# Kernel optimization log

Hardware: AMD Instinct MI355X
Metric: run time of the kernel (lower is better)

The kernel has to match this reference:

```python
import jax, jax.numpy as jnp
import numpy as np

LOC_SCOPE = 3.0
LOC_BIN_SIZE = 0.5
NUM_HEAD_BIN = 12
PER_LOC_BIN = int(LOC_SCOPE / LOC_BIN_SIZE) * 2  # 12
REG_C = PER_LOC_BIN * 4 + 1 + NUM_HEAD_BIN * 2 + 3  # 76


def decode_bbox_target(roi, reg, anchor):
    # roi: (M, 3) point centers; reg: (M, 76); anchor: (3,)
    b = PER_LOC_BIN
    f32 = reg.dtype
    x_bin = jnp.argmax(reg[:, 0:b], axis=1)
    z_bin = jnp.argmax(reg[:, b:2 * b], axis=1)
    pos_x = x_bin.astype(f32) * LOC_BIN_SIZE + LOC_BIN_SIZE / 2 - LOC_SCOPE
    pos_z = z_bin.astype(f32) * LOC_BIN_SIZE + LOC_BIN_SIZE / 2 - LOC_SCOPE
    # fine xz residual: gather residual of the argmax bin (batch_dims=1 gather)
    x_res = jnp.take_along_axis(reg[:, 2 * b:3 * b], x_bin[:, None], axis=1)[:, 0] * LOC_BIN_SIZE
    z_res = jnp.take_along_axis(reg[:, 3 * b:4 * b], z_bin[:, None], axis=1)[:, 0] * LOC_BIN_SIZE
    pos_x = pos_x + x_res
    pos_z = pos_z + z_res
    start = 4 * b
    # y by direct offset (get_y_by_bin=False)
    pos_y = roi[:, 1] + reg[:, start]
    start = start + 1
    # heading: coarse bin argmax + fine residual gather (get_ry_fine=False)
    ry_bin = jnp.argmax(reg[:, start:start + NUM_HEAD_BIN], axis=1)
    ry_res_norm = jnp.take_along_axis(
        reg[:, start + NUM_HEAD_BIN:start + 2 * NUM_HEAD_BIN], ry_bin[:, None], axis=1)[:, 0]
    angle_per_class = 2.0 * np.pi / NUM_HEAD_BIN
    ry = (ry_bin.astype(f32) * angle_per_class + ry_res_norm * (angle_per_class / 2)) % (2.0 * np.pi)
    ry = jnp.where(ry > np.pi, ry - 2.0 * np.pi, ry)
    # size: residual around anchor
    hwl = reg[:, start + 2 * NUM_HEAD_BIN:start + 2 * NUM_HEAD_BIN + 3] * anchor + anchor
    # roi has 3 cols -> no rotate_pc_along_y branch; shift x,z by roi center
    box = jnp.concatenate([
        (pos_x + roi[:, 0])[:, None],
        pos_y[:, None],
        (pos_z + roi[:, 2])[:, None],
        hwl,
        ry[:, None],
    ], axis=1)  # (M, 7)
    return box


def setup_inputs() -> dict:
    key = jax.random.key(0)
    k1, k2, k3 = jax.random.split(key, 3)
    B, N = 8, 131072
    rpn_scores = jax.random.normal(k1, (B, N), dtype=jnp.float32)
    rpn_reg = jax.random.normal(k2, (B, N, REG_C), dtype=jnp.float32)
    xyz = jax.random.normal(k3, (B, N, 3), dtype=jnp.float32) * 20.0
    anchor_size = jnp.array([1.52563191462, 1.62856739989, 3.88311640418], dtype=jnp.float32)
    return {"rpn_scores": rpn_scores, "rpn_reg": rpn_reg, "xyz": xyz, "anchor_size": anchor_size}


def reference(rpn_scores, rpn_reg, xyz, anchor_size):
    B, N, C = rpn_reg.shape
    props = decode_bbox_target(xyz.reshape(-1, 3), rpn_reg.reshape(-1, C), anchor_size)
    props = props.reshape(B, N, 7)
    # post_process: lift y to box top-center (y + h/2)
    props = jnp.concatenate([props[..., :1], props[..., 1:2] + props[..., 3:4] / 2, props[..., 2:]], axis=-1)
    # score-descending ordering of proposals (per batch row)
    order = jnp.argsort(-rpn_scores, axis=1)  # (B, N)
    boxes = jnp.take_along_axis(props, order[..., None], axis=1)
    scores = jnp.take_along_axis(rpn_scores, order, axis=1)
    # pack boxes+scores: (B, N, 8)
    return jnp.concatenate([boxes, scores[..., None]], axis=-1)
```

## Files before the change

### kernel.cpp

```cpp
#include <hip/hip_runtime.h>
#include <math.h>

#define N_PER   131072
#define NBATCH  8
#define REGC    76
#define TOTAL   (NBATCH * N_PER)
#define TILE    4096
#define NBLKSEG 32
#define BINS    256

__device__ __forceinline__ unsigned desc_key(float f) {
    unsigned u = __float_as_uint(f);
    return (u & 0x80000000u) ? u : ~(u | 0x80000000u);
}

__global__ __launch_bounds__(256) void decode_kernel(
    const float* __restrict__ scores, const float* __restrict__ reg,
    const float* __restrict__ xyz, const float* __restrict__ anchor,
    float* __restrict__ boxes8, unsigned* __restrict__ keyA,
    unsigned* __restrict__ payA)
{
    int p = blockIdx.x * 256 + threadIdx.x;
    const float* r = reg + (size_t)p * REGC;
    const float4* r4 = (const float4*)r;

    float4 q0 = r4[0],  q1 = r4[1],  q2 = r4[2];
    float4 q3 = r4[3],  q4 = r4[4],  q5 = r4[5];
    float4 s0 = r4[12], s1 = r4[13], s2 = r4[14], s3 = r4[15];
    float4 tt = r4[18];

    float xa[12] = {q0.x,q0.y,q0.z,q0.w, q1.x,q1.y,q1.z,q1.w, q2.x,q2.y,q2.z,q2.w};
    float za[12] = {q3.x,q3.y,q3.z,q3.w, q4.x,q4.y,q4.z,q4.w, q5.x,q5.y,q5.z,q5.w};
    float ra[12] = {s0.y,s0.z,s0.w, s1.x,s1.y,s1.z,s1.w, s2.x,s2.y,s2.z,s2.w, s3.x};

    int xb = 0; float xm = xa[0];
#pragma unroll
    for (int c = 1; c < 12; ++c) { if (xa[c] > xm) { xm = xa[c]; xb = c; } }
    int zb = 0; float zm = za[0];
#pragma unroll
    for (int c = 1; c < 12; ++c) { if (za[c] > zm) { zm = za[c]; zb = c; } }
    int yb = 0; float ym = ra[0];
#pragma unroll
    for (int c = 1; c < 12; ++c) { if (ra[c] > ym) { ym = ra[c]; yb = c; } }

    float x_res  = r[24 + xb];
    float z_res  = r[36 + zb];
    float ry_res = r[61 + yb];

    float rx = xyz[(size_t)p * 3 + 0];
    float ryy = xyz[(size_t)p * 3 + 1];
    float rz = xyz[(size_t)p * 3 + 2];
    float a0 = anchor[0], a1 = anchor[1], a2 = anchor[2];

    const float APC    = (float)(2.0 * M_PI / 12.0);
    const float HAPC   = (float)(M_PI / 12.0);
    const float TWO_PI = (float)(2.0 * M_PI);
    const float PI_F   = (float)M_PI;

    float vry = __fadd_rn(__fmul_rn((float)yb, APC), __fmul_rn(ry_res, HAPC));
    float m = fmodf(vry, TWO_PI);
    if (m < 0.0f) m += TWO_PI;
    if (m > PI_F) m -= TWO_PI;

    float h = tt.y * a0 + a0;
    float w = tt.z * a1 + a1;
    float l = tt.w * a2 + a2;

    float ox = (((float)xb * 0.5f + 0.25f - 3.0f) + x_res * 0.5f) + rx;
    float oz = (((float)zb * 0.5f + 0.25f - 3.0f) + z_res * 0.5f) + rz;
    float oy = (ryy + s0.x) + h * 0.5f;

    float sc = scores[p];

    float4* ob = (float4*)(boxes8 + (size_t)p * 8);
    ob[0] = make_float4(ox, oy, oz, h);
    ob[1] = make_float4(w, l, m, sc);

    keyA[p] = desc_key(sc);
    payA[p] = (unsigned)(p & (N_PER - 1));
}

__global__ __launch_bounds__(256) void hist_kernel(
    const unsigned* __restrict__ keyIn, unsigned* __restrict__ hist, int shift)
{
    __shared__ unsigned h[BINS];
    int tid = threadIdx.x;
    h[tid] = 0;
    __syncthreads();
    int seg = blockIdx.y, blk = blockIdx.x;
    const unsigned* k = keyIn + (size_t)seg * N_PER + (size_t)blk * TILE;
#pragma unroll
    for (int c = 0; c < TILE / 256; ++c) {
        unsigned d = (k[c * 256 + tid] >> shift) & 255u;
        atomicAdd(&h[d], 1u);
    }
    __syncthreads();
    hist[(size_t)(seg * BINS + tid) * NBLKSEG + blk] = h[tid];
}

__global__ __launch_bounds__(256) void scan_kernel(unsigned* __restrict__ hist)
{
    int seg = blockIdx.x, bin = threadIdx.x;
    unsigned* hp = hist + (size_t)(seg * BINS + bin) * NBLKSEG;
    unsigned run = 0;
#pragma unroll
    for (int blk = 0; blk < NBLKSEG; ++blk) {
        unsigned c = hp[blk];
        hp[blk] = run;
        run += c;
    }
    __shared__ unsigned sc[BINS];
    sc[bin] = run;
    __syncthreads();
    for (int off = 1; off < BINS; off <<= 1) {
        unsigned v = (bin >= off) ? sc[bin - off] : 0u;
        __syncthreads();
        sc[bin] += v;
        __syncthreads();
    }
    unsigned excl = sc[bin] - run;
#pragma unroll
    for (int blk = 0; blk < NBLKSEG; ++blk) hp[blk] += excl;
}

__global__ __launch_bounds__(256) void scatter_kernel(
    const unsigned* __restrict__ keyIn, const unsigned* __restrict__ payIn,
    unsigned* __restrict__ keyOut, unsigned* __restrict__ payOut,
    const unsigned* __restrict__ hist, int shift)
{
    __shared__ unsigned offs[BINS];
    __shared__ unsigned running[BINS];
    __shared__ unsigned whist[4][BINS];
    int tid = threadIdx.x;
    int seg = blockIdx.y, blk = blockIdx.x;
    int wave = tid >> 6, lane = tid & 63;
    unsigned long long lmask = (1ull << lane) - 1ull;

    offs[tid] = hist[(size_t)(seg * BINS + tid) * NBLKSEG + blk];
    running[tid] = 0;
#pragma unroll
    for (int w2 = 0; w2 < 4; ++w2) whist[w2][tid] = 0;

    const unsigned* ki = keyIn + (size_t)seg * N_PER + (size_t)blk * TILE;
    const unsigned* pi = payIn + (size_t)seg * N_PER + (size_t)blk * TILE;
    unsigned* ko = keyOut + (size_t)seg * N_PER;
    unsigned* po = payOut + (size_t)seg * N_PER;

    for (int c = 0; c < TILE / 256; ++c) {
        __syncthreads();
        unsigned key = ki[c * 256 + tid];
        unsigned pay = pi[c * 256 + tid];
        unsigned d = (key >> shift) & 255u;
        unsigned long long peers = ~0ull;
#pragma unroll
        for (int b = 0; b < 8; ++b) {
            unsigned long long vote = __ballot((d >> b) & 1u);
            peers &= ((d >> b) & 1u) ? vote : ~vote;
        }
        unsigned rank = (unsigned)__popcll(peers & lmask);
        unsigned cnt  = (unsigned)__popcll(peers);
        if (rank == 0) whist[wave][d] = cnt;
        __syncthreads();
        unsigned prefix = running[d];
#pragma unroll
        for (int w2 = 0; w2 < 4; ++w2) { if (w2 < wave) prefix += whist[w2][d]; }
        unsigned pos = offs[d] + prefix + rank;
        ko[pos] = key;
        po[pos] = pay;
        __syncthreads();
        unsigned sum = whist[0][tid] + whist[1][tid] + whist[2][tid] + whist[3][tid];
        running[tid] += sum;
        whist[0][tid] = 0; whist[1][tid] = 0; whist[2][tid] = 0; whist[3][tid] = 0;
    }
}

__global__ __launch_bounds__(256) void gather_kernel(
    const float* __restrict__ boxes8, const unsigned* __restrict__ pay,
    float* __restrict__ out)
{
    int g = blockIdx.x * 256 + threadIdx.x;
    int row = g >> 1, half = g & 1;
    int b = row >> 17;
    unsigned i = pay[row];
    const float4* src = (const float4*)(boxes8 + ((size_t)((b << 17) | (int)i)) * 8);
    float4 v = src[half];
    ((float4*)(out + (size_t)row * 8))[half] = v;
}

extern "C" void kernel_launch(void* const* d_in, const int* in_sizes, int n_in,
                              void* d_out, int out_size, void* d_ws, size_t ws_size,
                              hipStream_t stream)
{
    const float* scores = (const float*)d_in[0];
    const float* reg    = (const float*)d_in[1];
    const float* xyz    = (const float*)d_in[2];
    const float* anchor = (const float*)d_in[3];
    float* out = (float*)d_out;

    char* ws = (char*)d_ws;
    float*    boxes8 = (float*)ws;
    size_t    off    = (size_t)TOTAL * 8 * sizeof(float);
    unsigned* keyA = (unsigned*)(ws + off); off += (size_t)TOTAL * 4;
    unsigned* payA = (unsigned*)(ws + off); off += (size_t)TOTAL * 4;
    unsigned* keyB = (unsigned*)(ws + off); off += (size_t)TOTAL * 4;
    unsigned* payB = (unsigned*)(ws + off); off += (size_t)TOTAL * 4;
    unsigned* hist = (unsigned*)(ws + off); off += (size_t)NBATCH * BINS * NBLKSEG * 4;
    (void)ws_size; (void)in_sizes; (void)n_in; (void)out_size;

    decode_kernel<<<TOTAL / 256, 256, 0, stream>>>(scores, reg, xyz, anchor,
                                                   boxes8, keyA, payA);

    unsigned *ka = keyA, *pa = payA, *kb = keyB, *pb = payB;
    for (int pass = 0; pass < 4; ++pass) {
        int shift = pass * 8;
        hist_kernel<<<dim3(NBLKSEG, NBATCH), 256, 0, stream>>>(ka, hist, shift);
        scan_kernel<<<NBATCH, 256, 0, stream>>>(hist);
        scatter_kernel<<<dim3(NBLKSEG, NBATCH), 256, 0, stream>>>(ka, pa, kb, pb,
                                                                  hist, shift);
        unsigned* t;
        t = ka; ka = kb; kb = t;
        t = pa; pa = pb; pb = t;
    }

    gather_kernel<<<(TOTAL * 2) / 256, 256, 0, stream>>>(boxes8, pa, out);
}
```

Before: 588.8 us.

## Fuse histograms into decode/scatter, stage reg rows in LDS, fold gather into final scatter

Removes the four separate histogram kernels. Decode now computes the first-digit histogram with global atomics, and each scatter pass accumulates the next digit's histogram as it writes keys. The final scatter pass copies box rows straight into the output, which eliminates the separate gather kernel and the last key/payload write. Decode stages each 128-row block of reg into LDS with coalesced float4 loads instead of strided per-thread loads. The tile size is halved to give more blocks per segment. Global atomics on the histograms may contend, and the decode LDS footprint is large.

```diff
diff --git a/kernel.cpp b/kernel.cpp
--- a/kernel.cpp
+++ b/kernel.cpp
@@ -5,51 +5,56 @@
 #define NBATCH  8
 #define REGC    76
 #define TOTAL   (NBATCH * N_PER)
-#define TILE    4096
-#define NBLKSEG 32
+#define TILE    2048
+#define NBLKSEG 64
 #define BINS    256
+#define HISTW   (NBATCH * BINS * NBLKSEG)
 
 __device__ __forceinline__ unsigned desc_key(float f) {
     unsigned u = __float_as_uint(f);
     return (u & 0x80000000u) ? u : ~(u | 0x80000000u);
 }
 
-__global__ __launch_bounds__(256) void decode_kernel(
+__global__ __launch_bounds__(128) void decode_kernel(
     const float* __restrict__ scores, const float* __restrict__ reg,
     const float* __restrict__ xyz, const float* __restrict__ anchor,
     float* __restrict__ boxes8, unsigned* __restrict__ keyA,
-    unsigned* __restrict__ payA)
-{
-    int p = blockIdx.x * 256 + threadIdx.x;
-    const float* r = reg + (size_t)p * REGC;
-    const float4* r4 = (const float4*)r;
-
-    float4 q0 = r4[0],  q1 = r4[1],  q2 = r4[2];
-    float4 q3 = r4[3],  q4 = r4[4],  q5 = r4[5];
-    float4 s0 = r4[12], s1 = r4[13], s2 = r4[14], s3 = r4[15];
-    float4 tt = r4[18];
-
-    float xa[12] = {q0.x,q0.y,q0.z,q0.w, q1.x,q1.y,q1.z,q1.w, q2.x,q2.y,q2.z,q2.w};
-    float za[12] = {q3.x,q3.y,q3.z,q3.w, q4.x,q4.y,q4.z,q4.w, q5.x,q5.y,q5.z,q5.w};
-    float ra[12] = {s0.y,s0.z,s0.w, s1.x,s1.y,s1.z,s1.w, s2.x,s2.y,s2.z,s2.w, s3.x};
-
-    int xb = 0; float xm = xa[0];
-#pragma unroll
-    for (int c = 1; c < 12; ++c) { if (xa[c] > xm) { xm = xa[c]; xb = c; } }
-    int zb = 0; float zm = za[0];
-#pragma unroll
-    for (int c = 1; c < 12; ++c) { if (za[c] > zm) { zm = za[c]; zb = c; } }
-    int yb = 0; float ym = ra[0];
-#pragma unroll
-    for (int c = 1; c < 12; ++c) { if (ra[c] > ym) { ym = ra[c]; yb = c; } }
+    unsigned* __restrict__ payA, unsigned* __restrict__ hist0)
+{
+    __shared__ float lds[128 * 77];
+    int tid = threadIdx.x;
+    int p = blockIdx.x * 128 + tid;
+
+    const float4* g4 = (const float4*)(reg + (size_t)blockIdx.x * 128 * REGC);
+#pragma unroll
+    for (int j = 0; j < 19; ++j) {
+        int f = j * 128 + tid;
+        int row = f / 19, col = f - row * 19;
+        float4 v = g4[f];
+        float* dst = &lds[row * 77 + col * 4];
+        dst[0] = v.x; dst[1] = v.y; dst[2] = v.z; dst[3] = v.w;
+    }
+    __syncthreads();
+
+    const float* r = &lds[tid * 77];
+
+    int xb = 0; float xm = r[0];
+#pragma unroll
+    for (int c = 1; c < 12; ++c) { float v = r[c];      if (v > xm) { xm = v; xb = c; } }
+    int zb = 0; float zm = r[12];
+#pragma unroll
+    for (int c = 1; c < 12; ++c) { float v = r[12 + c]; if (v > zm) { zm = v; zb = c; } }
+    int yb = 0; float ym = r[49];
+#pragma unroll
+    for (int c = 1; c < 12; ++c) { float v = r[49 + c]; if (v > ym) { ym = v; yb = c; } }
 
     float x_res  = r[24 + xb];
     float z_res  = r[36 + zb];
     float ry_res = r[61 + yb];
 
-    float rx = xyz[(size_t)p * 3 + 0];
+    float rx  = xyz[(size_t)p * 3 + 0];
     float ryy = xyz[(size_t)p * 3 + 1];
-    float rz = xyz[(size_t)p * 3 + 2];
+    float rz  = xyz[(size_t)p * 3 + 2];
     float a0 = anchor[0], a1 = anchor[1], a2 = anchor[2];
 
     const float APC    = (float)(2.0 * M_PI / 12.0);
@@ -62,13 +67,13 @@
     if (m < 0.0f) m += TWO_PI;
     if (m > PI_F) m -= TWO_PI;
 
-    float h = tt.y * a0 + a0;
-    float w = tt.z * a1 + a1;
-    float l = tt.w * a2 + a2;
+    float h = r[73] * a0 + a0;
+    float w = r[74] * a1 + a1;
+    float l = r[75] * a2 + a2;
 
     float ox = (((float)xb * 0.5f + 0.25f - 3.0f) + x_res * 0.5f) + rx;
     float oz = (((float)zb * 0.5f + 0.25f - 3.0f) + z_res * 0.5f) + rz;
-    float oy = (ryy + s0.x) + h * 0.5f;
+    float oy = (ryy + r[48]) + h * 0.5f;
 
     float sc = scores[p];
 
@@ -76,38 +81,27 @@
     ob[0] = make_float4(ox, oy, oz, h);
     ob[1] = make_float4(w, l, m, sc);
 
-    keyA[p] = desc_key(sc);
+    unsigned key = desc_key(sc);
+    keyA[p] = key;
     payA[p] = (unsigned)(p & (N_PER - 1));
-}
-
-__global__ __launch_bounds__(256) void hist_kernel(
-    const unsigned* __restrict__ keyIn, unsigned* __restrict__ hist, int shift)
-{
-    __shared__ unsigned h[BINS];
-    int tid = threadIdx.x;
-    h[tid] = 0;
-    __syncthreads();
-    int seg = blockIdx.y, blk = blockIdx.x;
-    const unsigned* k = keyIn + (size_t)seg * N_PER + (size_t)blk * TILE;
-#pragma unroll
-    for (int c = 0; c < TILE / 256; ++c) {
-        unsigned d = (k[c * 256 + tid] >> shift) & 255u;
-        atomicAdd(&h[d], 1u);
-    }
-    __syncthreads();
-    hist[(size_t)(seg * BINS + tid) * NBLKSEG + blk] = h[tid];
+
+    int seg = p >> 17;
+    int blk = (p & (N_PER - 1)) >> 11;
+    atomicAdd(&hist0[(size_t)(seg * BINS + (key & 255u)) * NBLKSEG + blk], 1u);
 }
 
 __global__ __launch_bounds__(256) void scan_kernel(unsigned* __restrict__ hist)
 {
     int seg = blockIdx.x, bin = threadIdx.x;
-    unsigned* hp = hist + (size_t)(seg * BINS + bin) * NBLKSEG;
+    uint4* hp = (uint4*)(hist + (size_t)(seg * BINS + bin) * NBLKSEG);
     unsigned run = 0;
 #pragma unroll
-    for (int blk = 0; blk < NBLKSEG; ++blk) {
-        unsigned c = hp[blk];
-        hp[blk] = run;
-        run += c;
+    for (int i = 0; i < NBLKSEG / 4; ++i) {
+        uint4 v = hp[i];
+        uint4 o;
+        o.x = run; o.y = o.x + v.x; o.z = o.y + v.y; o.w = o.z + v.z;
+        run = o.w + v.w;
+        hp[i] = o;
     }
     __shared__ unsigned sc[BINS];
     sc[bin] = run;
@@ -120,13 +114,19 @@
     }
     unsigned excl = sc[bin] - run;
 #pragma unroll
-    for (int blk = 0; blk < NBLKSEG; ++blk) hp[blk] += excl;
-}
-
+    for (int i = 0; i < NBLKSEG / 4; ++i) {
+        uint4 o = hp[i];
+        o.x += excl; o.y += excl; o.z += excl; o.w += excl;
+        hp[i] = o;
+    }
+}
+
+template <int SHIFT, bool FINAL>
 __global__ __launch_bounds__(256) void scatter_kernel(
     const unsigned* __restrict__ keyIn, const unsigned* __restrict__ payIn,
     unsigned* __restrict__ keyOut, unsigned* __restrict__ payOut,
-    const unsigned* __restrict__ hist, int shift)
+    const unsigned* __restrict__ hist, unsigned* __restrict__ histNext,
+    const float* __restrict__ boxes8, float* __restrict__ out)
 {
     __shared__ unsigned offs[BINS];
     __shared__ unsigned running[BINS];
@@ -143,14 +143,12 @@
 
     const unsigned* ki = keyIn + (size_t)seg * N_PER + (size_t)blk * TILE;
     const unsigned* pi = payIn + (size_t)seg * N_PER + (size_t)blk * TILE;
-    unsigned* ko = keyOut + (size_t)seg * N_PER;
-    unsigned* po = payOut + (size_t)seg * N_PER;
 
     for (int c = 0; c < TILE / 256; ++c) {
         __syncthreads();
         unsigned key = ki[c * 256 + tid];
         unsigned pay = pi[c * 256 + tid];
-        unsigned d = (key >> shift) & 255u;
+        unsigned d = (key >> SHIFT) & 255u;
         unsigned long long peers = ~0ull;
 #pragma unroll
         for (int b = 0; b < 8; ++b) {
@@ -165,26 +163,26 @@
 #pragma unroll
         for (int w2 = 0; w2 < 4; ++w2) { if (w2 < wave) prefix += whist[w2][d]; }
         unsigned pos = offs[d] + prefix + rank;
-        ko[pos] = key;
-        po[pos] = pay;
+
+        if (FINAL) {
+            const float4* src = (const float4*)(boxes8 +
+                                ((size_t)(seg * N_PER) + pay) * 8);
+            float4 v0 = src[0], v1 = src[1];
+            float4* dst = (float4*)(out + ((size_t)(seg * N_PER) + pos) * 8);
+            dst[0] = v0; dst[1] = v1;
+        } else {
+            unsigned* ko = keyOut + (size_t)seg * N_PER;
+            unsigned* po = payOut + (size_t)seg * N_PER;
+            ko[pos] = key;
+            po[pos] = pay;
+            unsigned nd = (key >> (SHIFT + 8)) & 255u;
+            atomicAdd(&histNext[(size_t)(seg * BINS + nd) * NBLKSEG + (pos >> 11)], 1u);
+        }
         __syncthreads();
         unsigned sum = whist[0][tid] + whist[1][tid] + whist[2][tid] + whist[3][tid];
         running[tid] += sum;
         whist[0][tid] = 0; whist[1][tid] = 0; whist[2][tid] = 0; whist[3][tid] = 0;
     }
-}
-
-__global__ __launch_bounds__(256) void gather_kernel(
-    const float* __restrict__ boxes8, const unsigned* __restrict__ pay,
-    float* __restrict__ out)
-{
-    int g = blockIdx.x * 256 + threadIdx.x;
-    int row = g >> 1, half = g & 1;
-    int b = row >> 17;
-    unsigned i = pay[row];
-    const float4* src = (const float4*)(boxes8 + ((size_t)((b << 17) | (int)i)) * 8);
-    float4 v = src[half];
-    ((float4*)(out + (size_t)row * 8))[half] = v;
 }
 
 extern "C" void kernel_launch(void* const* d_in, const int* in_sizes, int n_in,
@@ -204,23 +202,29 @@
     unsigned* payA = (unsigned*)(ws + off); off += (size_t)TOTAL * 4;
     unsigned* keyB = (unsigned*)(ws + off); off += (size_t)TOTAL * 4;
     unsigned* payB = (unsigned*)(ws + off); off += (size_t)TOTAL * 4;
-    unsigned* hist = (unsigned*)(ws + off); off += (size_t)NBATCH * BINS * NBLKSEG * 4;
+    unsigned* histAll = (unsigned*)(ws + off); off += (size_t)4 * HISTW * 4;
+    unsigned* h0 = histAll;
+    unsigned* h1 = histAll + HISTW;
+    unsigned* h2 = histAll + 2 * (size_t)HISTW;
+    unsigned* h3 = histAll + 3 * (size_t)HISTW;
     (void)ws_size; (void)in_sizes; (void)n_in; (void)out_size;
 
-    decode_kernel<<<TOTAL / 256, 256, 0, stream>>>(scores, reg, xyz, anchor,
-                                                   boxes8, keyA, payA);
-
-    unsigned *ka = keyA, *pa = payA, *kb = keyB, *pb = payB;
-    for (int pass = 0; pass < 4; ++pass) {
-        int shift = pass * 8;
-        hist_kernel<<<dim3(NBLKSEG, NBATCH), 256, 0, stream>>>(ka, hist, shift);
-        scan_kernel<<<NBATCH, 256, 0, stream>>>(hist);
-        scatter_kernel<<<dim3(NBLKSEG, NBATCH), 256, 0, stream>>>(ka, pa, kb, pb,
-                                                                  hist, shift);
-        unsigned* t;
-        t = ka; ka = kb; kb = t;
-        t = pa; pa = pb; pb = t;
-    }
-
-    gather_kernel<<<(TOTAL * 2) / 256, 256, 0, stream>>>(boxes8, pa, out);
-}
+    hipMemsetAsync(histAll, 0, (size_t)4 * HISTW * 4, stream);
+
+    decode_kernel<<<TOTAL / 128, 128, 0, stream>>>(scores, reg, xyz, anchor,
+                                                   boxes8, keyA, payA, h0);
+
+    dim3 sg(NBLKSEG, NBATCH);
+    scan_kernel<<<NBATCH, 256, 0, stream>>>(h0);
+    scatter_kernel<0,  false><<<sg, 256, 0, stream>>>(keyA, payA, keyB, payB,
+                                                      h0, h1, nullptr, nullptr);
+    scan_kernel<<<NBATCH, 256, 0, stream>>>(h1);
+    scatter_kernel<8,  false><<<sg, 256, 0, stream>>>(keyB, payB, keyA, payA,
+                                                      h1, h2, nullptr, nullptr);
+    scan_kernel<<<NBATCH, 256, 0, stream>>>(h2);
+    scatter_kernel<16, false><<<sg, 256, 0, stream>>>(keyA, payA, keyB, payB,
+                                                      h2, h3, nullptr, nullptr);
+    scan_kernel<<<NBATCH, 256, 0, stream>>>(h3);
+    scatter_kernel<24, true ><<<sg, 256, 0, stream>>>(keyB, payB, nullptr, nullptr,
+                                                      h3, nullptr, boxes8, out);
+}
```

Result: slower. 705.2 us (+19.8%).
